# Kernel optimization log

Measured on AMD Instinct MI355X. Metric: run time of the kernel, lower is better.

Reference implementation:

```python
import jax, jax.numpy as jnp
import numpy as np

B, N, E, F_IN, F_OUT, HEADS, HDIM = 64, 1024, 16384, 300, 8, 4, 32
ALPHA = 0.5
BETA = float(np.log(0.1 / 2 + 1.0))  # GCN2Conv: theta=0.1, layer=2


def _norm(src, dst, ew, n):
    # GCN normalization with added self loops: D^-1/2 (A + I) D^-1/2, edge-list form
    idx = jnp.arange(n)
    r = jnp.concatenate([src, idx])
    c = jnp.concatenate([dst, idx])
    w = jnp.concatenate([ew, jnp.ones((n,), ew.dtype)])
    deg = jax.ops.segment_sum(w, c, num_segments=n)  # deg >= 1 (self loop weight 1)
    dinv = jax.lax.rsqrt(jnp.maximum(deg, 1e-12))
    return r, c, dinv[r] * w * dinv[c]


def _prop(h, r, c, w, n):
    # out[c] += w * h[r]  (source-to-target message passing)
    return jax.ops.segment_sum(w[:, None] * h[r], c, num_segments=n)


def _forward(edge_index, x, edge_weight, W1, b1, W2, b2, W3, b3, W4, b4, Wl, Wr, att, bg, Wg1, Wm, bm, Wg2, Wp1, bp1, Wp2, bp2, Wo, bo):
    def per_graph(xg, ei, ewg):
        src, dst = ei[0], ei[1]
        n = xg.shape[0]
        r, c, w = _norm(src, dst, ewg, n)                    # weighted gcn norm
        r1, c1, w1 = _norm(src, dst, jnp.ones_like(ewg), n)  # unweighted gcn norm
        h1 = jax.nn.relu(_prop(xg @ W1, r, c, w, n) + b1)    # [n,256]
        h2 = jax.nn.relu(_prop(h1 @ W2, r, c, w, n) + b2)    # [n,128]
        h = jax.nn.relu(_prop(h2 @ W3, r, c, w, n) + b3)     # [n,64]
        h = jax.nn.relu(_prop(h @ W4, r, c, w, n) + b4)      # [n,32]
        # GATv2Conv(32, 32, heads=4), self loops, concat heads, eval mode (no dropout)
        idx = jnp.arange(n)
        s2, d2 = jnp.concatenate([src, idx]), jnp.concatenate([dst, idx])
        xl = (h @ Wl).reshape(n, HEADS, HDIM)  # source transform
        xr = (h @ Wr).reshape(n, HEADS, HDIM)  # target transform
        e = jax.nn.leaky_relu(xl[s2] + xr[d2], 0.2)          # [E2,H,C]
        lg = jnp.einsum('ehc,hc->eh', e, att)                # [E2,H]
        mx = jax.ops.segment_max(lg, d2, num_segments=n)
        a = jnp.exp(lg - mx[d2])
        alpha = a / jax.ops.segment_sum(a, d2, num_segments=n)[d2]
        h = jax.ops.segment_sum(alpha[..., None] * xl[s2], d2, num_segments=n).reshape(n, HEADS * HDIM) + bg
        h = jax.nn.relu(h)                                   # [n,128]
        # GCN2Conv(128, alpha=0.5, theta=0.1, layer=2), x0 = h2, shared weights, no bias
        z = (1.0 - ALPHA) * _prop(h, r, c, w, n) + ALPHA * h2
        h = jax.nn.relu((1.0 - BETA) * z + BETA * (z @ Wg1))
        # GCNConv(128, 256) called WITHOUT edge weights
        h = jax.nn.relu(_prop(h @ Wm, r1, c1, w1, n) + bm)
        # GCN2Conv(256, 0.5, 0.1, 2), x0 = h1
        z = (1.0 - ALPHA) * _prop(h, r, c, w, n) + ALPHA * h1
        h = jax.nn.relu((1.0 - BETA) * z + BETA * (z @ Wg2))  # [n,256]
        # dense_diff_pool stage 1: GCNConv(256,5) soft assignments + to_dense_adj
        s = jax.nn.softmax(_prop(h @ Wp1, r, c, w, n) + bp1, axis=-1)  # [n,5]
        adj = jnp.zeros((n, n), h.dtype).at[src, dst].add(ewg)
        nodes = s.T @ h                                      # [5,256]
        adj2 = s.T @ adj @ s                                 # [5,5]
        # DenseGCNConv(256,1): set diag to 1, sym-normalize, propagate
        di = jnp.arange(5)
        adjl = adj2.at[di, di].set(1.0)
        dd = jax.lax.rsqrt(jnp.maximum(adjl.sum(-1), 1.0))
        sc = jax.nn.softmax((dd[:, None] * adjl * dd[None, :]) @ (nodes @ Wp2) + bp2, axis=-1)  # [5,1]
        # dense_diff_pool stage 2
        return (sc.T @ nodes)[0]                             # [256]

    pooled = jax.vmap(per_graph)(x, edge_index, edge_weight)  # [B,256]
    return pooled @ Wo + bo


def setup_inputs():
    key = jax.random.key(0)
    ks = jax.random.split(key, 32)
    lin = lambda k, fi, fo: jax.random.normal(k, (fi, fo), jnp.float32) / np.sqrt(fi)
    return {
        'x': jax.random.normal(ks[0], (B, N, F_IN), jnp.float32),
        'edge_index': jax.random.randint(ks[1], (B, 2, E), 0, N),
        'edge_weight': jax.random.uniform(ks[2], (B, E), jnp.float32),
        'W1': lin(ks[3], F_IN, 256), 'b1': jnp.zeros((256,), jnp.float32),
        'W2': lin(ks[4], 256, 128), 'b2': jnp.zeros((128,), jnp.float32),
        'W3': lin(ks[5], 128, 64), 'b3': jnp.zeros((64,), jnp.float32),
        'W4': lin(ks[6], 64, 32), 'b4': jnp.zeros((32,), jnp.float32),
        'Wl': lin(ks[7], 32, 128), 'Wr': lin(ks[8], 32, 128),
        'att': jax.random.normal(ks[9], (HEADS, HDIM), jnp.float32) / np.sqrt(HDIM),
        'bg': jnp.zeros((128,), jnp.float32),
        'Wg1': lin(ks[10], 128, 128),
        'Wm': lin(ks[11], 128, 256), 'bm': jnp.zeros((256,), jnp.float32),
        'Wg2': lin(ks[12], 256, 256),
        'Wp1': lin(ks[13], 256, 5), 'bp1': jnp.zeros((5,), jnp.float32),
        'Wp2': lin(ks[14], 256, 1), 'bp2': jnp.zeros((1,), jnp.float32),
        'Wo': lin(ks[15], 256, F_OUT), 'bo': jnp.zeros((F_OUT,), jnp.float32),
    }


def reference(x, edge_index, edge_weight, W1, b1, W2, b2, W3, b3, W4, b4, Wl, Wr, att, bg, Wg1, Wm, bm, Wg2, Wp1, bp1, Wp2, bp2, Wo, bo):
    return _forward(edge_index, x, edge_weight, W1, b1, W2, b2, W3, b3, W4, b4, Wl, Wr, att, bg, Wg1, Wm, bm, Wg2, Wp1, bp1, Wp2, bp2, Wo, bo)
```

## Files before the change

### kernel.cpp

```cpp
#include <hip/hip_runtime.h>
#include <cstdint>
#include <cstddef>

constexpr int NB = 64;
constexpr int NN = 1024;
constexpr int NE = 16384;
constexpr int NCH = 8;
constexpr int CHE = NE / NCH;
constexpr float C_BETA = 0.04879016417f;

typedef __attribute__((ext_vector_type(8))) short s8v;
typedef __attribute__((ext_vector_type(4))) float f4v;

__device__ inline float bf2f(ushort u){ union{uint u;float f;} v; v.u=((uint)u)<<16; return v.f; }
__device__ inline ushort f2bf(float f){ union{float f;uint u;} v; v.f=f; uint r=v.u+0x7fffu+((v.u>>16)&1u); return (ushort)(r>>16); }
__device__ inline void up8(uint4 x, float* o){
  o[0]=bf2f((ushort)x.x); o[1]=bf2f((ushort)(x.x>>16));
  o[2]=bf2f((ushort)x.y); o[3]=bf2f((ushort)(x.y>>16));
  o[4]=bf2f((ushort)x.z); o[5]=bf2f((ushort)(x.z>>16));
  o[6]=bf2f((ushort)x.w); o[7]=bf2f((ushort)(x.w>>16));
}
__device__ inline uint pk2(float a, float b){ return (uint)f2bf(a) | ((uint)f2bf(b)<<16); }
__device__ inline uint4 pk8(const float* f){
  uint4 v; v.x=pk2(f[0],f[1]); v.y=pk2(f[2],f[3]); v.z=pk2(f[4],f[5]); v.w=pk2(f[6],f[7]); return v;
}
__device__ inline int swz8(int bid, int bpg){
  int xcd = bid & 7, j = bid >> 3;
  return (xcd * (NB/8) + j / bpg) * bpg + (j % bpg);
}


__global__ __launch_bounds__(256) void hist_k(const int* __restrict__ ei,
    const float* __restrict__ ew, int* __restrict__ phist, float* __restrict__ pdegw) {
  int blk = blockIdx.x;
  int b = blk >> 3, ch = blk & 7;
  __shared__ int hc[NN];
  __shared__ float hw[NN];
  int t = threadIdx.x;
  for (int i = t; i < NN; i += 256) { hc[i] = 0; hw[i] = 0.f; }
  __syncthreads();
  const int* dstb = ei + (size_t)b * 2 * NE + NE + ch * CHE;
  const float* ewb = ew + (size_t)b * NE + ch * CHE;
  for (int e = t; e < CHE; e += 256) {
    int d = dstb[e];
    atomicAdd(&hc[d], 1);
    atomicAdd(&hw[d], ewb[e]);
  }
  __syncthreads();
  size_t o = ((size_t)b * NCH + ch) * NN;
  for (int i = t; i < NN; i += 256) {
    phist[o + i] = hc[i];
    pdegw[o + i] = hw[i];
  }
}

__global__ __launch_bounds__(1024) void scan2_k(int* __restrict__ phist,
    const float* __restrict__ pdegw, float* __restrict__ dinvw,
    float* __restrict__ dinvu, int* __restrict__ rowptr) {
  int b = blockIdx.x, t = threadIdx.x;
  size_t base = (size_t)b * NCH * NN;
  int h[NCH];
  int cnt = 0; float dw = 1.0f;
#pragma unroll
  for (int c = 0; c < NCH; ++c) {
    h[c] = phist[base + c * NN + t];
    cnt += h[c];
    dw += pdegw[base + c * NN + t];
  }
  dinvw[b * NN + t] = rsqrtf(dw);
  dinvu[b * NN + t] = rsqrtf(1.0f + (float)cnt);
  __shared__ int ss[NN];
  ss[t] = cnt;
  __syncthreads();
  for (int off = 1; off < NN; off <<= 1) {
    int xv = (t >= off) ? ss[t - off] : 0;
    __syncthreads();
    ss[t] += xv;
    __syncthreads();
  }
  rowptr[b * (NN + 1) + t + 1] = ss[t];
  if (t == 0) rowptr[b * (NN + 1)] = 0;
  int excl = ss[t] - cnt;
#pragma unroll
  for (int c = 0; c < NCH; ++c) {
    phist[base + c * NN + t] = excl;
    excl += h[c];
  }
}

__global__ __launch_bounds__(256) void scatter2_k(const int* __restrict__ ei,
    const float* __restrict__ ew, const int* __restrict__ coff,
    const float* __restrict__ dinvw, const float* __restrict__ dinvu,
    int2* __restrict__ peW, int2* __restrict__ peU) {
  int blk = blockIdx.x;
  int b = blk >> 3, ch = blk & 7;
  __shared__ int sbase[NN];
  __shared__ int sfill[NN];
  __shared__ float sdw[NN];
  __shared__ float sdu[NN];
  int t = threadIdx.x;
  for (int i = t; i < NN; i += 256) {
    sbase[i] = coff[((size_t)b * NCH + ch) * NN + i];
    sfill[i] = 0;
    sdw[i] = dinvw[b * NN + i];
    sdu[i] = dinvu[b * NN + i];
  }
  __syncthreads();
  const int* srcb = ei + (size_t)b * 2 * NE + ch * CHE;
  const int* dstb = ei + (size_t)b * 2 * NE + NE + ch * CHE;
  const float* ewb = ew + (size_t)b * NE + ch * CHE;
  int2* pwb = peW + (size_t)b * NE;
  int2* pub = peU + (size_t)b * NE;
  for (int e = t; e < CHE; e += 256) {
    int s = srcb[e], d = dstb[e];
    int pos = sbase[d] + atomicAdd(&sfill[d], 1);
    pwb[pos] = make_int2(s, __float_as_int(sdw[s] * ewb[e] * sdw[d]));
    pub[pos] = make_int2(s, __float_as_int(sdu[s] * sdu[d]));
  }
}


__device__ inline void wcv(const float* __restrict__ W, ushort* __restrict__ Wt,
                           int idx, int K, int N, int Kp) {
  int n = idx / Kp, k = idx % Kp;
  Wt[idx] = (k < K) ? f2bf(W[(size_t)k * N + n]) : (ushort)0;
}

__global__ void wconv_all_k(const float* W1, const float* W2, const float* W3,
                            const float* W4, const float* Wl, const float* Wr,
                            const float* Wg1, const float* Wm, const float* Wg2,
                            ushort* Wt1, ushort* Wt2, ushort* Wt3, ushort* Wt4,
                            ushort* WtLR, ushort* Wtg1, ushort* Wtm, ushort* Wtg2) {
  int bb = blockIdx.x, t = threadIdx.x;
  if      (bb < 320) wcv(W1, Wt1, bb * 256 + t, 300, 256, 320);
  else if (bb < 448) wcv(W2, Wt2, (bb - 320) * 256 + t, 256, 128, 256);
  else if (bb < 480) wcv(W3, Wt3, (bb - 448) * 256 + t, 128, 64, 128);
  else if (bb < 488) wcv(W4, Wt4, (bb - 480) * 256 + t, 64, 32, 64);
  else if (bb < 504) wcv(Wl, WtLR, (bb - 488) * 256 + t, 32, 128, 32);
  else if (bb < 520) wcv(Wr, WtLR + 128 * 32, (bb - 504) * 256 + t, 32, 128, 32);
  else if (bb < 584) wcv(Wg1, Wtg1, (bb - 520) * 256 + t, 128, 128, 128);
  else if (bb < 712) wcv(Wm, Wtm, (bb - 584) * 256 + t, 128, 256, 128);
  else               wcv(Wg2, Wtg2, (bb - 712) * 256 + t, 256, 256, 256);
}


template<int WR, int NI, int MODE, int AF32>
__global__ __launch_bounds__(256) void mgemm_k(const ushort* __restrict__ A,
    const float* __restrict__ Af, const ushort* __restrict__ Bt,
    const ushort* __restrict__ Z, ushort* __restrict__ C, int M, int K, int N) {
  constexpr int BM = WR * 32;
  constexpr int BN = NI * 32;
  constexpr int KR = 300;
  __shared__ ushort As[BM][40];
  __shared__ ushort Bs[BN][40];
  int tid = threadIdx.x;
  int wave = tid >> 6, lane = tid & 63;
  int bm = blockIdx.y * BM, bn = blockIdx.x * BN;
  int wm = (wave >> 1) * (WR * 16), wn = (wave & 1) * (NI * 16);
  f4v acc[WR][NI];
#pragma unroll
  for (int a = 0; a < WR; ++a)
#pragma unroll
    for (int b = 0; b < NI; ++b)
#pragma unroll
      for (int q = 0; q < 4; ++q) acc[a][b][q] = 0.f;
  int r = lane & 15, kg = (lane >> 4) * 8;
  for (int k0 = 0; k0 < K; k0 += 32) {
#pragma unroll
    for (int c = tid; c < BM * 4; c += 256) {
      int row = c >> 2, kc = (c & 3) * 8;
      if (AF32) {
        const float* xr = Af + (size_t)(bm + row) * KR + k0 + kc;
        float f[8];
        if (k0 + kc + 8 <= KR) {
          float4 a = *(const float4*)xr;
          float4 bq = *(const float4*)(xr + 4);
          f[0]=a.x; f[1]=a.y; f[2]=a.z; f[3]=a.w;
          f[4]=bq.x; f[5]=bq.y; f[6]=bq.z; f[7]=bq.w;
        } else {
#pragma unroll
          for (int j = 0; j < 8; ++j) f[j] = (k0 + kc + j < KR) ? xr[j] : 0.f;
        }
        *(uint4*)&As[row][kc] = pk8(f);
      } else {
        *(uint4*)&As[row][kc] = *(const uint4*)&A[(size_t)(bm + row) * K + k0 + kc];
      }
    }
#pragma unroll
    for (int c = tid; c < BN * 4; c += 256) {
      int col = c >> 2, kc = (c & 3) * 8;
      *(uint4*)&Bs[col][kc] = *(const uint4*)&Bt[(size_t)(bn + col) * K + k0 + kc];
    }
    __syncthreads();
    s8v af[WR], bf[NI];
#pragma unroll
    for (int mi = 0; mi < WR; ++mi) af[mi] = *(const s8v*)&As[wm + mi * 16 + r][kg];
#pragma unroll
    for (int ni = 0; ni < NI; ++ni) bf[ni] = *(const s8v*)&Bs[wn + ni * 16 + r][kg];
#pragma unroll
    for (int mi = 0; mi < WR; ++mi)
#pragma unroll
      for (int ni = 0; ni < NI; ++ni)
        acc[mi][ni] = __builtin_amdgcn_mfma_f32_16x16x32_bf16(af[mi], bf[ni], acc[mi][ni], 0, 0, 0);
    __syncthreads();
  }
  int col = lane & 15, rowg = (lane >> 4) * 4;
#pragma unroll
  for (int mi = 0; mi < WR; ++mi)
#pragma unroll
    for (int ni = 0; ni < NI; ++ni)
#pragma unroll
      for (int q = 0; q < 4; ++q) {
        int row = bm + wm + mi * 16 + rowg + q;
        int cc = bn + wn + ni * 16 + col;
        size_t idx = (size_t)row * N + cc;
        float v = acc[mi][ni][q];
        if (MODE == 2) v = fmaxf((1.f - C_BETA) * bf2f(Z[idx]) + C_BETA * v, 0.f);
        C[idx] = f2bf(v);
      }
}


template<int D, int MODE>
__global__ __launch_bounds__(256) void prop_k(const ushort* __restrict__ in,
    ushort* __restrict__ out, const int2* __restrict__ pedge,
    const float* __restrict__ dinv, const int* __restrict__ rowptr,
    const float* __restrict__ bias, const ushort* __restrict__ x0) {
  constexpr int TPN = D / 8, NPB = 256 / TPN, BPG = NN / NPB;
  int t = threadIdx.x;
  int bid = swz8(blockIdx.x, BPG);
  int tn = t / TPN, cl = t % TPN;
  int node = bid * NPB + tn;
  int b = node >> 10, i = node & 1023;
  float di = dinv[node];
  float f[8], acc[8];
  uint4 ov = *(const uint4*)&in[(size_t)node * D + cl * 8];
  up8(ov, f);
  float w0 = di * di;
#pragma unroll
  for (int j = 0; j < 8; ++j) acc[j] = w0 * f[j];
  int r0 = rowptr[b * (NN + 1) + i], r1 = rowptr[b * (NN + 1) + i + 1];
  const int2* pe = pedge + (size_t)b * NE;
  const ushort* inb = in + (size_t)b * NN * D;
  int p = r0;
  for (; p + 4 <= r1; p += 4) {
    int2 e0 = pe[p], e1 = pe[p + 1], e2 = pe[p + 2], e3 = pe[p + 3];
    float wa = __int_as_float(e0.y);
    float wb2 = __int_as_float(e1.y);
    float wc = __int_as_float(e2.y);
    float wd = __int_as_float(e3.y);
    uint4 rv0 = *(const uint4*)&inb[(size_t)e0.x * D + cl * 8];
    uint4 rv1 = *(const uint4*)&inb[(size_t)e1.x * D + cl * 8];
    uint4 rv2 = *(const uint4*)&inb[(size_t)e2.x * D + cl * 8];
    uint4 rv3 = *(const uint4*)&inb[(size_t)e3.x * D + cl * 8];
    up8(rv0, f);
#pragma unroll
    for (int j = 0; j < 8; ++j) acc[j] += wa * f[j];
    up8(rv1, f);
#pragma unroll
    for (int j = 0; j < 8; ++j) acc[j] += wb2 * f[j];
    up8(rv2, f);
#pragma unroll
    for (int j = 0; j < 8; ++j) acc[j] += wc * f[j];
    up8(rv3, f);
#pragma unroll
    for (int j = 0; j < 8; ++j) acc[j] += wd * f[j];
  }
  for (; p < r1; ++p) {
    int2 e = pe[p];
    float w = __int_as_float(e.y);
    uint4 rv = *(const uint4*)&inb[(size_t)e.x * D + cl * 8];
    up8(rv, f);
#pragma unroll
    for (int j = 0; j < 8; ++j) acc[j] += w * f[j];
  }
  size_t ob = (size_t)node * D + cl * 8;
  if (MODE == 0) {
#pragma unroll
    for (int j = 0; j < 8; ++j) acc[j] = fmaxf(acc[j] + bias[cl * 8 + j], 0.f);
  } else {
    uint4 xv = *(const uint4*)&x0[ob];
    up8(xv, f);
#pragma unroll
    for (int j = 0; j < 8; ++j) acc[j] = 0.5f * acc[j] + 0.5f * f[j];
  }
  *(uint4*)&out[ob] = pk8(acc);
}


#define GAT_UPD(P, FL)                                            \
  if (P > m + 8.f) {                           \
    float sc = __expf(m - P);                                     \
    den *= sc;                                                    \
    _Pragma("unroll")                                             \
    for (int j = 0; j < 8; ++j) acc[j] *= sc;                     \
    m = P;                                                        \
    den += 1.f;                                                   \
    _Pragma("unroll")                                             \
    for (int j = 0; j < 8; ++j) acc[j] += FL[j];                  \
  } else {                                                        \
    float ex = __expf(P - m);                                     \
    den += ex;                                                    \
    _Pragma("unroll")                                             \
    for (int j = 0; j < 8; ++j) acc[j] += ex * FL[j];             \
  }

__global__ __launch_bounds__(256) void gat_fused_k(const ushort* __restrict__ xlr,
    const int2* __restrict__ pedge, const int* __restrict__ rowptr,
    const float* __restrict__ att, const float* __restrict__ bg,
    ushort* __restrict__ out) {
  int bid = swz8(blockIdx.x, NN / 16);
  int t = threadIdx.x;
  int tn = t >> 4, cl = t & 15;
  int node = bid * 16 + tn;
  int b = node >> 10, i = node & 1023;
  int ch = cl * 8;
  int r0 = rowptr[b * (NN + 1) + i], r1 = rowptr[b * (NN + 1) + i + 1];
  const ushort* xb = xlr + (size_t)b * NN * 256;
  const int2* pe = pedge + (size_t)b * NE;
  float fr[8], at[8];
  {
    uint4 rv = *(const uint4*)&xb[(size_t)i * 256 + 128 + ch];
    up8(rv, fr);
#pragma unroll
    for (int j = 0; j < 8; ++j) at[j] = att[ch + j];
  }
  float m, den, acc[8];
  {
    float fs[8];
    uint4 sv = *(const uint4*)&xb[(size_t)i * 256 + ch];
    up8(sv, fs);
    float part = 0.f;
#pragma unroll
    for (int j = 0; j < 8; ++j) {
      float v = fs[j] + fr[j];
      part += fmaxf(v, 0.2f * v) * at[j];
    }
    part += __shfl_xor(part, 1);
    part += __shfl_xor(part, 2);
    m = part; den = 1.f;
#pragma unroll
    for (int j = 0; j < 8; ++j) acc[j] = fs[j];
  }
  float fl0[8], fl1[8];
  int p = r0;
  for (; p + 2 <= r1; p += 2) {
    int s0 = pe[p].x, s1 = pe[p + 1].x;
    uint4 v0 = *(const uint4*)&xb[(size_t)s0 * 256 + ch];
    uint4 v1 = *(const uint4*)&xb[(size_t)s1 * 256 + ch];
    up8(v0, fl0); up8(v1, fl1);
    float p0 = 0.f, p1 = 0.f;
#pragma unroll
    for (int j = 0; j < 8; ++j) {
      float a0 = fl0[j] + fr[j];
      float a1 = fl1[j] + fr[j];
      p0 += fmaxf(a0, 0.2f * a0) * at[j];
      p1 += fmaxf(a1, 0.2f * a1) * at[j];
    }
    p0 += __shfl_xor(p0, 1); p0 += __shfl_xor(p0, 2);
    p1 += __shfl_xor(p1, 1); p1 += __shfl_xor(p1, 2);
    GAT_UPD(p0, fl0)
    GAT_UPD(p1, fl1)
  }
  if (p < r1) {
    int s = pe[p].x;
    uint4 v0 = *(const uint4*)&xb[(size_t)s * 256 + ch];
    up8(v0, fl0);
    float p0 = 0.f;
#pragma unroll
    for (int j = 0; j < 8; ++j) {
      float a0 = fl0[j] + fr[j];
      p0 += fmaxf(a0, 0.2f * a0) * at[j];
    }
    p0 += __shfl_xor(p0, 1); p0 += __shfl_xor(p0, 2);
    GAT_UPD(p0, fl0)
  }
  float inv = 1.f / den;
#pragma unroll
  for (int j = 0; j < 8; ++j) acc[j] = fmaxf(acc[j] * inv + bg[ch + j], 0.f);
  *(uint4*)&out[(size_t)node * 128 + ch] = pk8(acc);
}


__global__ __launch_bounds__(256) void pool_part_k(const ushort* __restrict__ h7,
                                                   float* __restrict__ part) {
  int bid = blockIdx.x;
  int bgr = bid >> 3, seg = bid & 7;
  int t = threadIdx.x;
  int rg = t >> 5, cl = t & 31;
  const ushort* hb = h7 + (size_t)bgr * NN * 256;
  float a[8] = {};
  float f[8];
  for (int r = seg * 128 + rg; r < seg * 128 + 128; r += 8) {
    uint4 v = *(const uint4*)&hb[(size_t)r * 256 + cl * 8];
    up8(v, f);
#pragma unroll
    for (int j = 0; j < 8; ++j) a[j] += f[j];
  }
  __shared__ float red[8][256];
#pragma unroll
  for (int j = 0; j < 8; ++j) red[rg][cl * 8 + j] = a[j];
  __syncthreads();
  float s = 0.f;
#pragma unroll
  for (int g = 0; g < 8; ++g) s += red[g][t];
  part[(size_t)bid * 256 + t] = s;
}

__global__ __launch_bounds__(256) void pool_out_k(const float* __restrict__ part,
    const float* __restrict__ Wo, const float* __restrict__ bo, float* __restrict__ out) {
  int bgr = blockIdx.x, t = threadIdx.x;
  float s = 0.f;
#pragma unroll
  for (int g = 0; g < 8; ++g) s += part[(size_t)(bgr * 8 + g) * 256 + t];
  __shared__ float pv[256];
  pv[t] = s;
  __syncthreads();
  if (t < 8) {
    float o = bo[t];
    for (int c = 0; c < 256; ++c) o += pv[c] * Wo[c * 8 + t];
    out[bgr * 8 + t] = o;
  }
}

__global__ void zero_out_k(float* out, int n) {
  int g = blockIdx.x * 256 + threadIdx.x;
  if (g < n) out[g] = 0.f;
}


extern "C" void kernel_launch(void* const* d_in, const int* in_sizes, int n_in,
                              void* d_out, int out_size, void* d_ws, size_t ws_size,
                              hipStream_t stream) {
  const float* x   = (const float*)d_in[0];
  const int*   ei  = (const int*)d_in[1];
  const float* ew  = (const float*)d_in[2];
  const float* W1  = (const float*)d_in[3];
  const float* b1  = (const float*)d_in[4];
  const float* W2  = (const float*)d_in[5];
  const float* b2  = (const float*)d_in[6];
  const float* W3  = (const float*)d_in[7];
  const float* b3  = (const float*)d_in[8];
  const float* W4  = (const float*)d_in[9];
  const float* b4  = (const float*)d_in[10];
  const float* Wl  = (const float*)d_in[11];
  const float* Wr  = (const float*)d_in[12];
  const float* att = (const float*)d_in[13];
  const float* bg  = (const float*)d_in[14];
  const float* Wg1 = (const float*)d_in[15];
  const float* Wm  = (const float*)d_in[16];
  const float* bm  = (const float*)d_in[17];
  const float* Wg2 = (const float*)d_in[18];
  const float* Wo  = (const float*)d_in[23];
  const float* bo  = (const float*)d_in[24];
  float* out = (float*)d_out;

  const int M = NB * NN;

  char* wp = (char*)d_ws;
  size_t used = 0;
  auto alloc = [&](size_t bytes) -> void* {
    void* p = (void*)wp;
    size_t a = (bytes + 255) & ~(size_t)255;
    wp += a; used += a;
    return p;
  };
  float* dinvw = (float*)alloc((size_t)NB * NN * 4);
  float* dinvu = (float*)alloc((size_t)NB * NN * 4);
  int*   rowptr= (int*)alloc((size_t)NB * (NN + 1) * 4);
  int*   phist = (int*)alloc((size_t)NB * NCH * NN * 4);
  float* pdegw = (float*)alloc((size_t)NB * NCH * NN * 4);
  int2*  peW   = (int2*)alloc((size_t)NB * NE * 8);
  int2*  peU   = (int2*)alloc((size_t)NB * NE * 8);
  float* part  = (float*)alloc((size_t)NB * 8 * 256 * 4);
  ushort* Wt1  = (ushort*)alloc((size_t)256 * 320 * 2);
  ushort* Wt2  = (ushort*)alloc((size_t)128 * 256 * 2);
  ushort* Wt3  = (ushort*)alloc((size_t)64 * 128 * 2);
  ushort* Wt4  = (ushort*)alloc((size_t)32 * 64 * 2);
  ushort* WtLR = (ushort*)alloc((size_t)256 * 32 * 2);
  ushort* Wtg1 = (ushort*)alloc((size_t)128 * 128 * 2);
  ushort* Wtm  = (ushort*)alloc((size_t)256 * 128 * 2);
  ushort* Wtg2 = (ushort*)alloc((size_t)256 * 256 * 2);
  ushort* B1 = (ushort*)alloc((size_t)M * 256 * 2);
  ushort* B2 = (ushort*)alloc((size_t)M * 256 * 2);
  ushort* B3 = (ushort*)alloc((size_t)M * 256 * 2);
  ushort* B4 = (ushort*)alloc((size_t)M * 256 * 2);
  ushort* B2a = B2, *B2b = B2 + (size_t)M * 128;
  ushort* B3a = B3, *B3b = B3 + (size_t)M * 128;

  if (used > ws_size) {
    zero_out_k<<<(out_size + 255) / 256, 256, 0, stream>>>(out, out_size);
    return;
  }

  hist_k<<<NB * NCH, 256, 0, stream>>>(ei, ew, phist, pdegw);
  scan2_k<<<NB, 1024, 0, stream>>>(phist, pdegw, dinvw, dinvu, rowptr);
  scatter2_k<<<NB * NCH, 256, 0, stream>>>(ei, ew, phist, dinvw, dinvu, peW, peU);

  wconv_all_k<<<968, 256, 0, stream>>>(W1, W2, W3, W4, Wl, Wr, Wg1, Wm, Wg2,
                                       Wt1, Wt2, Wt3, Wt4, WtLR, Wtg1, Wtm, Wtg2);

  mgemm_k<2,4,0,1><<<dim3(2, M / 64), 256, 0, stream>>>(nullptr, x, Wt1, nullptr, B2, M, 320, 256);
  prop_k<256,0><<<M / 8, 256, 0, stream>>>(B2, B1, peW, dinvw, rowptr, b1, nullptr);
  mgemm_k<2,4,0,0><<<dim3(1, M / 64), 256, 0, stream>>>(B1, nullptr, Wt2, nullptr, B2a, M, 256, 128);
  prop_k<128,0><<<M / 16, 256, 0, stream>>>(B2a, B3a, peW, dinvw, rowptr, b2, nullptr);
  mgemm_k<2,2,0,0><<<dim3(1, M / 64), 256, 0, stream>>>(B3a, nullptr, Wt3, nullptr, B2a, M, 128, 64);
  prop_k<64,0><<<M / 32, 256, 0, stream>>>(B2a, B3b, peW, dinvw, rowptr, b3, nullptr);
  mgemm_k<2,1,0,0><<<dim3(1, M / 64), 256, 0, stream>>>(B3b, nullptr, Wt4, nullptr, B2a, M, 64, 32);
  prop_k<32,0><<<M / 64, 256, 0, stream>>>(B2a, B2b, peW, dinvw, rowptr, b4, nullptr);

  mgemm_k<2,4,0,0><<<dim3(2, M / 64), 256, 0, stream>>>(B2b, nullptr, WtLR, nullptr, B4, M, 32, 256);
  gat_fused_k<<<M / 16, 256, 0, stream>>>(B4, peW, rowptr, att, bg, B2a);

  prop_k<128,1><<<M / 16, 256, 0, stream>>>(B2a, B2b, peW, dinvw, rowptr, nullptr, B3a);
  mgemm_k<2,4,2,0><<<dim3(1, M / 64), 256, 0, stream>>>(B2b, nullptr, Wtg1, B2b, B2a, M, 128, 128);

  mgemm_k<2,4,0,0><<<dim3(2, M / 64), 256, 0, stream>>>(B2a, nullptr, Wtm, nullptr, B3, M, 128, 256);
  prop_k<256,0><<<M / 8, 256, 0, stream>>>(B3, B2, peU, dinvu, rowptr, bm, nullptr);

  prop_k<256,1><<<M / 8, 256, 0, stream>>>(B2, B3, peW, dinvw, rowptr, nullptr, B1);
  mgemm_k<2,4,2,0><<<dim3(2, M / 64), 256, 0, stream>>>(B3, nullptr, Wtg2, B3, B2, M, 256, 256);

  pool_part_k<<<NB * 8, 256, 0, stream>>>(B2, part);
  pool_out_k<<<NB, 256, 0, stream>>>(part, Wo, bo, out);
}
```

Measured before the change: 429.5 us.

## Widen per-thread channels in prop kernels and pre-convert input to bf16

The propagation kernel gains a channels-per-thread parameter, so each thread now gathers 16 channels (two 16-byte loads per neighbour) for the wider layers. This halves the number of threads per node and the repeated edge-list and rowptr reads, at the cost of more registers and fewer blocks. A separate kernel converts the fp32 input x to padded bf16 once, which removes the fp32-to-bf16 path from the first GEMM's tile loading but adds an extra pass through memory. Weight conversion is moved ahead of the graph preprocessing kernels.

```diff
diff --git a/kernel.cpp b/kernel.cpp
--- a/kernel.cpp
+++ b/kernel.cpp
@@ -120,6 +120,23 @@
 }
 
 
+__global__ void xconv_k(const float* __restrict__ x, ushort* __restrict__ xbf) {
+  int g = blockIdx.x * 256 + threadIdx.x;
+  int row = g / 40, c = (g % 40) * 8;
+  float f[8];
+  const float* xr = x + (size_t)row * 300;
+  if (c + 8 <= 300) {
+    float4 a = *(const float4*)&xr[c];
+    float4 bq = *(const float4*)&xr[c + 4];
+    f[0]=a.x; f[1]=a.y; f[2]=a.z; f[3]=a.w;
+    f[4]=bq.x; f[5]=bq.y; f[6]=bq.z; f[7]=bq.w;
+  } else {
+#pragma unroll
+    for (int j = 0; j < 8; ++j) f[j] = (c + j < 300) ? xr[c + j] : 0.f;
+  }
+  *(uint4*)&xbf[(size_t)row * 320 + c] = pk8(f);
+}
+
 __device__ inline void wcv(const float* __restrict__ W, ushort* __restrict__ Wt,
                            int idx, int K, int N, int Kp) {
   int n = idx / Kp, k = idx % Kp;
@@ -144,13 +161,12 @@
 }
 
 
-template<int WR, int NI, int MODE, int AF32>
+template<int WR, int NI, int MODE>
 __global__ __launch_bounds__(256) void mgemm_k(const ushort* __restrict__ A,
-    const float* __restrict__ Af, const ushort* __restrict__ Bt,
-    const ushort* __restrict__ Z, ushort* __restrict__ C, int M, int K, int N) {
+    const ushort* __restrict__ Bt, const ushort* __restrict__ Z,
+    ushort* __restrict__ C, int M, int K, int N) {
   constexpr int BM = WR * 32;
   constexpr int BN = NI * 32;
-  constexpr int KR = 300;
   __shared__ ushort As[BM][40];
   __shared__ ushort Bs[BN][40];
   int tid = threadIdx.x;
@@ -169,22 +185,7 @@
 #pragma unroll
     for (int c = tid; c < BM * 4; c += 256) {
       int row = c >> 2, kc = (c & 3) * 8;
-      if (AF32) {
-        const float* xr = Af + (size_t)(bm + row) * KR + k0 + kc;
-        float f[8];
-        if (k0 + kc + 8 <= KR) {
-          float4 a = *(const float4*)xr;
-          float4 bq = *(const float4*)(xr + 4);
-          f[0]=a.x; f[1]=a.y; f[2]=a.z; f[3]=a.w;
-          f[4]=bq.x; f[5]=bq.y; f[6]=bq.z; f[7]=bq.w;
-        } else {
-#pragma unroll
-          for (int j = 0; j < 8; ++j) f[j] = (k0 + kc + j < KR) ? xr[j] : 0.f;
-        }
-        *(uint4*)&As[row][kc] = pk8(f);
-      } else {
-        *(uint4*)&As[row][kc] = *(const uint4*)&A[(size_t)(bm + row) * K + k0 + kc];
-      }
+      *(uint4*)&As[row][kc] = *(const uint4*)&A[(size_t)(bm + row) * K + k0 + kc];
     }
 #pragma unroll
     for (int c = tid; c < BN * 4; c += 256) {
@@ -221,70 +222,84 @@
 }
 
 
-template<int D, int MODE>
+template<int D, int MODE, int CPT>
 __global__ __launch_bounds__(256) void prop_k(const ushort* __restrict__ in,
     ushort* __restrict__ out, const int2* __restrict__ pedge,
     const float* __restrict__ dinv, const int* __restrict__ rowptr,
     const float* __restrict__ bias, const ushort* __restrict__ x0) {
-  constexpr int TPN = D / 8, NPB = 256 / TPN, BPG = NN / NPB;
+  constexpr int TPN = D / CPT, NPB = 256 / TPN, BPG = NN / NPB;
+  constexpr int NV = CPT / 8;
   int t = threadIdx.x;
   int bid = swz8(blockIdx.x, BPG);
   int tn = t / TPN, cl = t % TPN;
   int node = bid * NPB + tn;
   int b = node >> 10, i = node & 1023;
   float di = dinv[node];
-  float f[8], acc[8];
-  uint4 ov = *(const uint4*)&in[(size_t)node * D + cl * 8];
-  up8(ov, f);
+  float f[8], acc[CPT];
+  const ushort* selfp = &in[(size_t)node * D + cl * CPT];
   float w0 = di * di;
 #pragma unroll
-  for (int j = 0; j < 8; ++j) acc[j] = w0 * f[j];
+  for (int v = 0; v < NV; ++v) {
+    uint4 ov = *(const uint4*)&selfp[v * 8];
+    up8(ov, f);
+#pragma unroll
+    for (int j = 0; j < 8; ++j) acc[v * 8 + j] = w0 * f[j];
+  }
   int r0 = rowptr[b * (NN + 1) + i], r1 = rowptr[b * (NN + 1) + i + 1];
   const int2* pe = pedge + (size_t)b * NE;
-  const ushort* inb = in + (size_t)b * NN * D;
+  const ushort* inb = in + (size_t)b * NN * D + cl * CPT;
   int p = r0;
   for (; p + 4 <= r1; p += 4) {
-    int2 e0 = pe[p], e1 = pe[p + 1], e2 = pe[p + 2], e3 = pe[p + 3];
-    float wa = __int_as_float(e0.y);
-    float wb2 = __int_as_float(e1.y);
-    float wc = __int_as_float(e2.y);
-    float wd = __int_as_float(e3.y);
-    uint4 rv0 = *(const uint4*)&inb[(size_t)e0.x * D + cl * 8];
-    uint4 rv1 = *(const uint4*)&inb[(size_t)e1.x * D + cl * 8];
-    uint4 rv2 = *(const uint4*)&inb[(size_t)e2.x * D + cl * 8];
-    uint4 rv3 = *(const uint4*)&inb[(size_t)e3.x * D + cl * 8];
-    up8(rv0, f);
-#pragma unroll
-    for (int j = 0; j < 8; ++j) acc[j] += wa * f[j];
-    up8(rv1, f);
-#pragma unroll
-    for (int j = 0; j < 8; ++j) acc[j] += wb2 * f[j];
-    up8(rv2, f);
-#pragma unroll
-    for (int j = 0; j < 8; ++j) acc[j] += wc * f[j];
-    up8(rv3, f);
-#pragma unroll
-    for (int j = 0; j < 8; ++j) acc[j] += wd * f[j];
+    int2 ee[4]; uint4 rv[4][NV];
+#pragma unroll
+    for (int q = 0; q < 4; ++q) ee[q] = pe[p + q];
+#pragma unroll
+    for (int q = 0; q < 4; ++q)
+#pragma unroll
+      for (int v = 0; v < NV; ++v)
+        rv[q][v] = *(const uint4*)&inb[(size_t)ee[q].x * D + v * 8];
+#pragma unroll
+    for (int q = 0; q < 4; ++q) {
+      float w = __int_as_float(ee[q].y);
+#pragma unroll
+      for (int v = 0; v < NV; ++v) {
+        up8(rv[q][v], f);
+#pragma unroll
+        for (int j = 0; j < 8; ++j) acc[v * 8 + j] += w * f[j];
+      }
+    }
   }
   for (; p < r1; ++p) {
     int2 e = pe[p];
     float w = __int_as_float(e.y);
-    uint4 rv = *(const uint4*)&inb[(size_t)e.x * D + cl * 8];
-    up8(rv, f);
-#pragma unroll
-    for (int j = 0; j < 8; ++j) acc[j] += w * f[j];
-  }
-  size_t ob = (size_t)node * D + cl * 8;
+#pragma unroll
+    for (int v = 0; v < NV; ++v) {
+      uint4 rvv = *(const uint4*)&inb[(size_t)e.x * D + v * 8];
+      up8(rvv, f);
+#pragma unroll
+      for (int j = 0; j < 8; ++j) acc[v * 8 + j] += w * f[j];
+    }
+  }
+  size_t ob = (size_t)node * D + cl * CPT;
   if (MODE == 0) {
 #pragma unroll
-    for (int j = 0; j < 8; ++j) acc[j] = fmaxf(acc[j] + bias[cl * 8 + j], 0.f);
+    for (int v = 0; v < NV; ++v) {
+      float o8[8];
+#pragma unroll
+      for (int j = 0; j < 8; ++j) o8[j] = fmaxf(acc[v * 8 + j] + bias[cl * CPT + v * 8 + j], 0.f);
+      *(uint4*)&out[ob + v * 8] = pk8(o8);
+    }
   } else {
-    uint4 xv = *(const uint4*)&x0[ob];
-    up8(xv, f);
-#pragma unroll
-    for (int j = 0; j < 8; ++j) acc[j] = 0.5f * acc[j] + 0.5f * f[j];
-  }
-  *(uint4*)&out[ob] = pk8(acc);
+#pragma unroll
+    for (int v = 0; v < NV; ++v) {
+      uint4 xv = *(const uint4*)&x0[ob + v * 8];
+      up8(xv, f);
+      float o8[8];
+#pragma unroll
+      for (int j = 0; j < 8; ++j) o8[j] = 0.5f * acc[v * 8 + j] + 0.5f * f[j];
+      *(uint4*)&out[ob + v * 8] = pk8(o8);
+    }
+  }
 }
 
 
@@ -473,6 +488,7 @@
   int2*  peW   = (int2*)alloc((size_t)NB * NE * 8);
   int2*  peU   = (int2*)alloc((size_t)NB * NE * 8);
   float* part  = (float*)alloc((size_t)NB * 8 * 256 * 4);
+  ushort* xbf  = (ushort*)alloc((size_t)M * 320 * 2);
   ushort* Wt1  = (ushort*)alloc((size_t)256 * 320 * 2);
   ushort* Wt2  = (ushort*)alloc((size_t)128 * 256 * 2);
   ushort* Wt3  = (ushort*)alloc((size_t)64 * 128 * 2);
@@ -493,33 +509,34 @@
     return;
   }
 
+  wconv_all_k<<<968, 256, 0, stream>>>(W1, W2, W3, W4, Wl, Wr, Wg1, Wm, Wg2,
+                                       Wt1, Wt2, Wt3, Wt4, WtLR, Wtg1, Wtm, Wtg2);
+  xconv_k<<<M * 40 / 256, 256, 0, stream>>>(x, xbf);
+
   hist_k<<<NB * NCH, 256, 0, stream>>>(ei, ew, phist, pdegw);
   scan2_k<<<NB, 1024, 0, stream>>>(phist, pdegw, dinvw, dinvu, rowptr);
   scatter2_k<<<NB * NCH, 256, 0, stream>>>(ei, ew, phist, dinvw, dinvu, peW, peU);
 
-  wconv_all_k<<<968, 256, 0, stream>>>(W1, W2, W3, W4, Wl, Wr, Wg1, Wm, Wg2,
-                                       Wt1, Wt2, Wt3, Wt4, WtLR, Wtg1, Wtm, Wtg2);
-
-  mgemm_k<2,4,0,1><<<dim3(2, M / 64), 256, 0, stream>>>(nullptr, x, Wt1, nullptr, B2, M, 320, 256);
-  prop_k<256,0><<<M / 8, 256, 0, stream>>>(B2, B1, peW, dinvw, rowptr, b1, nullptr);
-  mgemm_k<2,4,0,0><<<dim3(1, M / 64), 256, 0, stream>>>(B1, nullptr, Wt2, nullptr, B2a, M, 256, 128);
-  prop_k<128,0><<<M / 16, 256, 0, stream>>>(B2a, B3a, peW, dinvw, rowptr, b2, nullptr);
-  mgemm_k<2,2,0,0><<<dim3(1, M / 64), 256, 0, stream>>>(B3a, nullptr, Wt3, nullptr, B2a, M, 128, 64);
-  prop_k<64,0><<<M / 32, 256, 0, stream>>>(B2a, B3b, peW, dinvw, rowptr, b3, nullptr);
-  mgemm_k<2,1,0,0><<<dim3(1, M / 64), 256, 0, stream>>>(B3b, nullptr, Wt4, nullptr, B2a, M, 64, 32);
-  prop_k<32,0><<<M / 64, 256, 0, stream>>>(B2a, B2b, peW, dinvw, rowptr, b4, nullptr);
-
-  mgemm_k<2,4,0,0><<<dim3(2, M / 64), 256, 0, stream>>>(B2b, nullptr, WtLR, nullptr, B4, M, 32, 256);
+  mgemm_k<2,4,0><<<dim3(2, M / 64), 256, 0, stream>>>(xbf, Wt1, nullptr, B2, M, 320, 256);
+  prop_k<256,0,16><<<M / 16, 256, 0, stream>>>(B2, B1, peW, dinvw, rowptr, b1, nullptr);
+  mgemm_k<2,4,0><<<dim3(1, M / 64), 256, 0, stream>>>(B1, Wt2, nullptr, B2a, M, 256, 128);
+  prop_k<128,0,16><<<M / 32, 256, 0, stream>>>(B2a, B3a, peW, dinvw, rowptr, b2, nullptr);
+  mgemm_k<2,2,0><<<dim3(1, M / 64), 256, 0, stream>>>(B3a, Wt3, nullptr, B2a, M, 128, 64);
+  prop_k<64,0,8><<<M / 32, 256, 0, stream>>>(B2a, B3b, peW, dinvw, rowptr, b3, nullptr);
+  mgemm_k<2,1,0><<<dim3(1, M / 64), 256, 0, stream>>>(B3b, Wt4, nullptr, B2a, M, 64, 32);
+  prop_k<32,0,8><<<M / 64, 256, 0, stream>>>(B2a, B2b, peW, dinvw, rowptr, b4, nullptr);
+
+  mgemm_k<2,4,0><<<dim3(2, M / 64), 256, 0, stream>>>(B2b, WtLR, nullptr, B4, M, 32, 256);
   gat_fused_k<<<M / 16, 256, 0, stream>>>(B4, peW, rowptr, att, bg, B2a);
 
-  prop_k<128,1><<<M / 16, 256, 0, stream>>>(B2a, B2b, peW, dinvw, rowptr, nullptr, B3a);
-  mgemm_k<2,4,2,0><<<dim3(1, M / 64), 256, 0, stream>>>(B2b, nullptr, Wtg1, B2b, B2a, M, 128, 128);
-
-  mgemm_k<2,4,0,0><<<dim3(2, M / 64), 256, 0, stream>>>(B2a, nullptr, Wtm, nullptr, B3, M, 128, 256);
-  prop_k<256,0><<<M / 8, 256, 0, stream>>>(B3, B2, peU, dinvu, rowptr, bm, nullptr);
-
-  prop_k<256,1><<<M / 8, 256, 0, stream>>>(B2, B3, peW, dinvw, rowptr, nullptr, B1);
-  mgemm_k<2,4,2,0><<<dim3(2, M / 64), 256, 0, stream>>>(B3, nullptr, Wtg2, B3, B2, M, 256, 256);
+  prop_k<128,1,16><<<M / 32, 256, 0, stream>>>(B2a, B2b, peW, dinvw, rowptr, nullptr, B3a);
+  mgemm_k<2,4,2><<<dim3(1, M / 64), 256, 0, stream>>>(B2b, Wtg1, B2b, B2a, M, 128, 128);
+
+  mgemm_k<2,4,0><<<dim3(2, M / 64), 256, 0, stream>>>(B2a, Wtm, nullptr, B3, M, 128, 256);
+  prop_k<256,0,16><<<M / 16, 256, 0, stream>>>(B3, B2, peU, dinvu, rowptr, bm, nullptr);
+
+  prop_k<256,1,16><<<M / 16, 256, 0, stream>>>(B2, B3, peW, dinvw, rowptr, nullptr, B1);
+  mgemm_k<2,4,2><<<dim3(2, M / 64), 256, 0, stream>>>(B3, Wtg2, B3, B2, M, 256, 256);
 
   pool_part_k<<<NB * 8, 256, 0, stream>>>(B2, part);
   pool_out_k<<<NB, 256, 0, stream>>>(part, Wo, bo, out);
```

New measurement: 469.4 us. 1.09x slower.

## Drop unweighted edge array; compute unweighted norm weights on the fly in prop

Applied to the files above, without the earlier changes.

Removes the separate peU edge list built in scatter, so the unweighted propagation reuses peW's source indices and computes each weight as dinvu[src]*dinvu[dst] inside prop_k. This cuts scatter write traffic and the shared dinvu table. The change also doubles the histogram/scatter chunk count to 16 with batch-minor block mapping, and moves the weight conversion kernel ahead of graph preprocessing. The trade-off is an extra gather of dinvu per edge in one prop layer.

```diff
diff --git a/kernel.cpp b/kernel.cpp
--- a/kernel.cpp
+++ b/kernel.cpp
@@ -5,7 +5,7 @@
 constexpr int NB = 64;
 constexpr int NN = 1024;
 constexpr int NE = 16384;
-constexpr int NCH = 8;
+constexpr int NCH = 16;
 constexpr int CHE = NE / NCH;
 constexpr float C_BETA = 0.04879016417f;
 
@@ -33,7 +33,7 @@
 __global__ __launch_bounds__(256) void hist_k(const int* __restrict__ ei,
     const float* __restrict__ ew, int* __restrict__ phist, float* __restrict__ pdegw) {
   int blk = blockIdx.x;
-  int b = blk >> 3, ch = blk & 7;
+  int b = blk & 63, ch = blk >> 6;
   __shared__ int hc[NN];
   __shared__ float hw[NN];
   int t = threadIdx.x;
@@ -90,32 +90,27 @@
 
 __global__ __launch_bounds__(256) void scatter2_k(const int* __restrict__ ei,
     const float* __restrict__ ew, const int* __restrict__ coff,
-    const float* __restrict__ dinvw, const float* __restrict__ dinvu,
-    int2* __restrict__ peW, int2* __restrict__ peU) {
+    const float* __restrict__ dinvw, int2* __restrict__ peW) {
   int blk = blockIdx.x;
-  int b = blk >> 3, ch = blk & 7;
+  int b = blk & 63, ch = blk >> 6;
   __shared__ int sbase[NN];
   __shared__ int sfill[NN];
   __shared__ float sdw[NN];
-  __shared__ float sdu[NN];
   int t = threadIdx.x;
   for (int i = t; i < NN; i += 256) {
     sbase[i] = coff[((size_t)b * NCH + ch) * NN + i];
     sfill[i] = 0;
     sdw[i] = dinvw[b * NN + i];
-    sdu[i] = dinvu[b * NN + i];
   }
   __syncthreads();
   const int* srcb = ei + (size_t)b * 2 * NE + ch * CHE;
   const int* dstb = ei + (size_t)b * 2 * NE + NE + ch * CHE;
   const float* ewb = ew + (size_t)b * NE + ch * CHE;
   int2* pwb = peW + (size_t)b * NE;
-  int2* pub = peU + (size_t)b * NE;
   for (int e = t; e < CHE; e += 256) {
     int s = srcb[e], d = dstb[e];
     int pos = sbase[d] + atomicAdd(&sfill[d], 1);
     pwb[pos] = make_int2(s, __float_as_int(sdw[s] * ewb[e] * sdw[d]));
-    pub[pos] = make_int2(s, __float_as_int(sdu[s] * sdu[d]));
   }
 }
 
@@ -221,7 +216,7 @@
 }
 
 
-template<int D, int MODE>
+template<int D, int MODE, int WSEL>
 __global__ __launch_bounds__(256) void prop_k(const ushort* __restrict__ in,
     ushort* __restrict__ out, const int2* __restrict__ pedge,
     const float* __restrict__ dinv, const int* __restrict__ rowptr,
@@ -241,14 +236,19 @@
   for (int j = 0; j < 8; ++j) acc[j] = w0 * f[j];
   int r0 = rowptr[b * (NN + 1) + i], r1 = rowptr[b * (NN + 1) + i + 1];
   const int2* pe = pedge + (size_t)b * NE;
+  const float* dvb = dinv + b * NN;
   const ushort* inb = in + (size_t)b * NN * D;
   int p = r0;
   for (; p + 4 <= r1; p += 4) {
     int2 e0 = pe[p], e1 = pe[p + 1], e2 = pe[p + 2], e3 = pe[p + 3];
-    float wa = __int_as_float(e0.y);
-    float wb2 = __int_as_float(e1.y);
-    float wc = __int_as_float(e2.y);
-    float wd = __int_as_float(e3.y);
+    float wa, wb2, wc, wd;
+    if (WSEL == 0) {
+      wa = __int_as_float(e0.y); wb2 = __int_as_float(e1.y);
+      wc = __int_as_float(e2.y); wd = __int_as_float(e3.y);
+    } else {
+      wa = dvb[e0.x] * di; wb2 = dvb[e1.x] * di;
+      wc = dvb[e2.x] * di; wd = dvb[e3.x] * di;
+    }
     uint4 rv0 = *(const uint4*)&inb[(size_t)e0.x * D + cl * 8];
     uint4 rv1 = *(const uint4*)&inb[(size_t)e1.x * D + cl * 8];
     uint4 rv2 = *(const uint4*)&inb[(size_t)e2.x * D + cl * 8];
@@ -268,7 +268,7 @@
   }
   for (; p < r1; ++p) {
     int2 e = pe[p];
-    float w = __int_as_float(e.y);
+    float w = (WSEL == 0) ? __int_as_float(e.y) : dvb[e.x] * di;
     uint4 rv = *(const uint4*)&inb[(size_t)e.x * D + cl * 8];
     up8(rv, f);
 #pragma unroll
@@ -471,7 +471,6 @@
   int*   phist = (int*)alloc((size_t)NB * NCH * NN * 4);
   float* pdegw = (float*)alloc((size_t)NB * NCH * NN * 4);
   int2*  peW   = (int2*)alloc((size_t)NB * NE * 8);
-  int2*  peU   = (int2*)alloc((size_t)NB * NE * 8);
   float* part  = (float*)alloc((size_t)NB * 8 * 256 * 4);
   ushort* Wt1  = (ushort*)alloc((size_t)256 * 320 * 2);
   ushort* Wt2  = (ushort*)alloc((size_t)128 * 256 * 2);
@@ -493,32 +492,32 @@
     return;
   }
 
+  wconv_all_k<<<968, 256, 0, stream>>>(W1, W2, W3, W4, Wl, Wr, Wg1, Wm, Wg2,
+                                       Wt1, Wt2, Wt3, Wt4, WtLR, Wtg1, Wtm, Wtg2);
+
   hist_k<<<NB * NCH, 256, 0, stream>>>(ei, ew, phist, pdegw);
   scan2_k<<<NB, 1024, 0, stream>>>(phist, pdegw, dinvw, dinvu, rowptr);
-  scatter2_k<<<NB * NCH, 256, 0, stream>>>(ei, ew, phist, dinvw, dinvu, peW, peU);
-
-  wconv_all_k<<<968, 256, 0, stream>>>(W1, W2, W3, W4, Wl, Wr, Wg1, Wm, Wg2,
-                                       Wt1, Wt2, Wt3, Wt4, WtLR, Wtg1, Wtm, Wtg2);
+  scatter2_k<<<NB * NCH, 256, 0, stream>>>(ei, ew, phist, dinvw, peW);
 
   mgemm_k<2,4,0,1><<<dim3(2, M / 64), 256, 0, stream>>>(nullptr, x, Wt1, nullptr, B2, M, 320, 256);
-  prop_k<256,0><<<M / 8, 256, 0, stream>>>(B2, B1, peW, dinvw, rowptr, b1, nullptr);
+  prop_k<256,0,0><<<M / 8, 256, 0, stream>>>(B2, B1, peW, dinvw, rowptr, b1, nullptr);
   mgemm_k<2,4,0,0><<<dim3(1, M / 64), 256, 0, stream>>>(B1, nullptr, Wt2, nullptr, B2a, M, 256, 128);
-  prop_k<128,0><<<M / 16, 256, 0, stream>>>(B2a, B3a, peW, dinvw, rowptr, b2, nullptr);
+  prop_k<128,0,0><<<M / 16, 256, 0, stream>>>(B2a, B3a, peW, dinvw, rowptr, b2, nullptr);
   mgemm_k<2,2,0,0><<<dim3(1, M / 64), 256, 0, stream>>>(B3a, nullptr, Wt3, nullptr, B2a, M, 128, 64);
-  prop_k<64,0><<<M / 32, 256, 0, stream>>>(B2a, B3b, peW, dinvw, rowptr, b3, nullptr);
+  prop_k<64,0,0><<<M / 32, 256, 0, stream>>>(B2a, B3b, peW, dinvw, rowptr, b3, nullptr);
   mgemm_k<2,1,0,0><<<dim3(1, M / 64), 256, 0, stream>>>(B3b, nullptr, Wt4, nullptr, B2a, M, 64, 32);
-  prop_k<32,0><<<M / 64, 256, 0, stream>>>(B2a, B2b, peW, dinvw, rowptr, b4, nullptr);
+  prop_k<32,0,0><<<M / 64, 256, 0, stream>>>(B2a, B2b, peW, dinvw, rowptr, b4, nullptr);
 
   mgemm_k<2,4,0,0><<<dim3(2, M / 64), 256, 0, stream>>>(B2b, nullptr, WtLR, nullptr, B4, M, 32, 256);
   gat_fused_k<<<M / 16, 256, 0, stream>>>(B4, peW, rowptr, att, bg, B2a);
 
-  prop_k<128,1><<<M / 16, 256, 0, stream>>>(B2a, B2b, peW, dinvw, rowptr, nullptr, B3a);
+  prop_k<128,1,0><<<M / 16, 256, 0, stream>>>(B2a, B2b, peW, dinvw, rowptr, nullptr, B3a);
   mgemm_k<2,4,2,0><<<dim3(1, M / 64), 256, 0, stream>>>(B2b, nullptr, Wtg1, B2b, B2a, M, 128, 128);
 
   mgemm_k<2,4,0,0><<<dim3(2, M / 64), 256, 0, stream>>>(B2a, nullptr, Wtm, nullptr, B3, M, 128, 256);
-  prop_k<256,0><<<M / 8, 256, 0, stream>>>(B3, B2, peU, dinvu, rowptr, bm, nullptr);
-
-  prop_k<256,1><<<M / 8, 256, 0, stream>>>(B2, B3, peW, dinvw, rowptr, nullptr, B1);
+  prop_k<256,0,1><<<M / 8, 256, 0, stream>>>(B3, B2, peW, dinvu, rowptr, bm, nullptr);
+
+  prop_k<256,1,0><<<M / 8, 256, 0, stream>>>(B2, B3, peW, dinvw, rowptr, nullptr, B1);
   mgemm_k<2,4,2,0><<<dim3(2, M / 64), 256, 0, stream>>>(B3, nullptr, Wtg2, B3, B2, M, 256, 256);
 
   pool_part_k<<<NB * 8, 256, 0, stream>>>(B2, part);
```

After: 415.5 us (median of 2 runs). -3.3%, faster.
